# Performance work log

Hardware: AMD Instinct MI355X
Metric: run time of the kernel (lower is better)

The kernel has to match this reference:

```python
import jax, jax.numpy as jnp
import numpy as np

V, E, H, C = 50000, 300, 512, 3
B, P_LEN, H_LEN = 64, 128, 64


def _lstm(x, Wih, Whh, bih, bhh, h0, c0):
    """torch-style LSTM (gate order i,f,g,o). x: [B,T,E] -> outputs [B,T,H], hT, cT."""
    def step(carry, xt):
        h, c = carry
        g = xt @ Wih.T + h @ Whh.T + bih + bhh  # [B,4H]
        i, f, gg, o = jnp.split(g, 4, axis=-1)
        c = jax.nn.sigmoid(f) * c + jax.nn.sigmoid(i) * jnp.tanh(gg)
        h = jax.nn.sigmoid(o) * jnp.tanh(c)
        return (h, c), h
    (hT, cT), ys = jax.lax.scan(step, (h0, c0), jnp.swapaxes(x, 0, 1))
    return jnp.swapaxes(ys, 0, 1), hT, cT


def setup_inputs() -> dict:
    key = jax.random.key(0)
    ks = iter(jax.random.split(key, 32))
    n = lambda shape, s=0.05: jax.random.normal(next(ks), shape, dtype=jnp.float32) * s
    inp = {
        "premise": jax.random.randint(next(ks), (B, P_LEN), 0, V, dtype=jnp.int32),
        "hypothesis": jax.random.randint(next(ks), (B, H_LEN), 0, V, dtype=jnp.int32),
        "emb": n((V, E), 0.1),
        "Wih1": n((4 * H, E)), "Whh1": n((4 * H, H)), "bih1": n((4 * H,)), "bhh1": n((4 * H,)),
        "Wih2": n((4 * H, E)), "Whh2": n((4 * H, H)), "bih2": n((4 * H,)), "bhh2": n((4 * H,)),
        "W_y": n((H, H)), "W_h": n((H, H)), "W_r": n((H, H)), "W_t": n((H, H)),
        "w_att": n((1, H)),
        "fc1_w": n((H, H)), "fc1_b": n((H,)),
        "fc2_w": n((H, H)), "fc2_b": n((H,)),
        "fc3_w": n((C, H)), "fc3_b": n((C,)),
    }
    return inp


def reference(premise, hypothesis, emb,
              Wih1, Whh1, bih1, bhh1,
              Wih2, Whh2, bih2, bhh2,
              W_y, W_h, W_r, W_t, w_att,
              fc1_w, fc1_b, fc2_w, fc2_b, fc3_w, fc3_b):
    Bsz = premise.shape[0]
    Hd = Whh1.shape[1]
    zeros = jnp.zeros((Bsz, Hd), jnp.float32)

    # premise LSTM
    xp = emb[premise]                                   # [B,P,E]
    out_p, _, c_p = _lstm(xp, Wih1, Whh1, bih1, bhh1, zeros, zeros)
    # hypothesis LSTM initialized with (h0=0, c0=c_p)
    xh = emb[hypothesis]                                # [B,Th,E]
    out_h, hn_h, _ = _lstm(xh, Wih2, Whh2, bih2, bhh2, zeros, c_p)

    # word-by-word attention: a1 = W_y @ V^T, fixed across steps
    a1 = jnp.einsum('hj,bpj->bhp', W_y, out_p)          # [B,H,P]
    wv = w_att[0]                                       # [H]

    def att_step(r, q_t):
        # r: [B,H] attention state; q_t: [B,H] hypothesis step
        a2 = q_t @ W_h.T + r @ W_r.T                    # [B,H]
        s = jnp.einsum('h,bhp->bp', wv, jnp.tanh(a1 + a2[:, :, None]))
        scores = jax.nn.softmax(s, axis=-1)             # over premise positions
        r = jnp.einsum('bph,bp->bh', out_p, scores) + jnp.tanh(r @ W_t.T)
        return r, None

    r, _ = jax.lax.scan(att_step, zeros, jnp.swapaxes(out_h, 0, 1))

    rep = jnp.tanh(r @ fc1_w.T + fc1_b + hn_h @ fc2_w.T + fc2_b)
    return rep @ fc3_w.T + fc3_b                         # [B,C]
```

## Files before the change

kernel.cpp:

```cpp
#include <hip/hip_runtime.h>
#include <math.h>

#define BSZ 64
#define PLEN 128
#define HLEN 64
#define EDIM 300
#define HDIM 512
#define G4 2048
#define NCLS 3

#define TOFF 1000u
#define SPIN_CAP (1 << 18)

#define CR16 576
#define C16(f) ((((f) >> 5) * 36) + ((f) & 31))

__device__ __forceinline__ float sigf(float x) { return 1.0f / (1.0f + __expf(-x)); }
__device__ __forceinline__ float tanhfast(float x) { return 1.0f - 2.0f / (__expf(2.0f * x) + 1.0f); }

__device__ __forceinline__ unsigned long long aload64(const unsigned long long* p) {
    return __hip_atomic_load(p, __ATOMIC_RELAXED, __HIP_MEMORY_SCOPE_AGENT);
}
__device__ __forceinline__ void astore64(unsigned long long* p, unsigned long long v) {
    __hip_atomic_store(p, v, __ATOMIC_RELAXED, __HIP_MEMORY_SCOPE_AGENT);
}
__device__ __forceinline__ unsigned long long tpack(float v, unsigned tag) {
    return ((unsigned long long)tag << 32) | (unsigned long long)__float_as_uint(v);
}
__device__ __forceinline__ float tval(unsigned long long v) { return __uint_as_float((unsigned)v); }
__device__ __forceinline__ unsigned ttag(unsigned long long v) { return (unsigned)(v >> 32); }

__global__ __launch_bounds__(256) void ws_zero(unsigned long long* p) {
    p[(size_t)blockIdx.x * 256 + threadIdx.x] = 0ull;
}

__global__ __launch_bounds__(256) void proj_kernel(
    const int* __restrict__ toks, const float* __restrict__ emb,
    const float* __restrict__ Wih, const float* __restrict__ bih,
    const float* __restrict__ bhh, float* __restrict__ out)
{
    __shared__ float es[32 * 100];
    __shared__ float wsh[64 * 100];
    __shared__ int tks[32];
    const int m0 = blockIdx.x * 32, r0 = blockIdx.y * 64;
    const int tid = threadIdx.x;
    const int tx = tid & 15, ty = tid >> 4;
    float acc[2][4] = {{0.f, 0.f, 0.f, 0.f}, {0.f, 0.f, 0.f, 0.f}};
    if (tid < 32) tks[tid] = toks[m0 + tid];
    __syncthreads();
    for (int kc = 0; kc < 3; kc++) {
        if (kc) __syncthreads();
        for (int i = tid; i < 800; i += 256) {
            int row = i / 25, k4 = i % 25;
            ((float4*)es)[i] = ((const float4*)(emb + (size_t)tks[row] * EDIM + kc * 100))[k4];
        }
        for (int i = tid; i < 1600; i += 256) {
            int row = i / 25, k4 = i % 25;
            ((float4*)wsh)[i] = ((const float4*)(Wih + (size_t)(r0 + row) * EDIM + kc * 100))[k4];
        }
        __syncthreads();
        const float4* e0 = (const float4*)es + ty * 25;
        const float4* e1 = e0 + 16 * 25;
        const float4* w0 = (const float4*)wsh + tx * 25;
#pragma unroll
        for (int k = 0; k < 25; k++) {
            float4 ea = e0[k], eb = e1[k];
#pragma unroll
            for (int j = 0; j < 4; j++) {
                float4 w = w0[k + j * 400];
                acc[0][j] += ea.x * w.x + ea.y * w.y + ea.z * w.z + ea.w * w.w;
                acc[1][j] += eb.x * w.x + eb.y * w.y + eb.z * w.z + eb.w * w.w;
            }
        }
    }
#pragma unroll
    for (int j = 0; j < 4; j++) {
        int rr = r0 + tx + j * 16;
        float bsum = bih[rr] + bhh[rr];
        out[(size_t)(m0 + ty) * G4 + rr]      = acc[0][j] + bsum;
        out[(size_t)(m0 + ty + 16) * G4 + rr] = acc[1][j] + bsum;
    }
}

__global__ __launch_bounds__(256, 1) void lstm_coop(
    const float* __restrict__ xp, const float* __restrict__ xh,
    const float* __restrict__ Whh1, const float* __restrict__ Whh2,
    float* __restrict__ outp, float* __restrict__ outh,
    unsigned long long* __restrict__ hA, unsigned long long* __restrict__ hB,
    unsigned long long* __restrict__ hC, unsigned long long* __restrict__ hD)
{
    const int tid = threadIdx.x;
    const int ug = blockIdx.x >> 3;
    const int bg = blockIdx.x & 7;
    const int u0 = ug * 16, b0 = bg * 8;
    const int rq = tid >> 4, cc = tid & 15;

    __shared__ __align__(16) float hst[8 * CR16];
    __shared__ float gsm[64][9];

    float4 w4[32];
#pragma unroll
    for (int j = 0; j < 4; j++) {
        int rr = 4 * rq + j;
        const float4* src = (const float4*)(Whh1 +
            ((size_t)((rr >> 4) * HDIM + u0 + (rr & 15))) * HDIM) + cc * 8;
#pragma unroll
        for (int q = 0; q < 8; q++) w4[j * 8 + q] = src[q];
    }
    float creg = 0.0f;
    const int bbc = tid >> 4, uuc = tid & 15;

    for (int t = 0; t < PLEN + HLEN; t++) {
        const int layer2 = (t >= PLEN) ? 1 : 0;
        const int tloc = layer2 ? t - PLEN : t;
        const int T = layer2 ? HLEN : PLEN;
        const float* xproj = layer2 ? xh : xp;
        float* outseq = layer2 ? outh : outp;
        unsigned long long* wA = layer2 ? hC : hA;
        unsigned long long* wB = layer2 ? hD : hB;
        unsigned long long* hwr = (t & 1) ? wB : wA;
        const unsigned long long* hrd = (t & 1) ? wA : wB;

        float gi = 0.f, gf = 0.f, gg = 0.f, go = 0.f;
        if (tid < 128) {
            size_t xb = ((size_t)(b0 + bbc) * T + tloc) * G4 + u0 + uuc;
            gi = xproj[xb];        gf = xproj[xb + 512];
            gg = xproj[xb + 1024]; go = xproj[xb + 1536];
        }

        if (t == PLEN) {
#pragma unroll
            for (int j = 0; j < 4; j++) {
                int rr = 4 * rq + j;
                const float4* src = (const float4*)(Whh2 +
                    ((size_t)((rr >> 4) * HDIM + u0 + (rr & 15))) * HDIM) + cc * 8;
#pragma unroll
                for (int q = 0; q < 8; q++) w4[j * 8 + q] = src[q];
            }
        }
        const bool have_h = (tloc != 0);
        if (have_h) {
            const unsigned long long* src = hrd + (size_t)b0 * 512;
            unsigned long long v[16];
            const unsigned expt = (unsigned)t;
#pragma unroll
            for (int i = 0; i < 16; i++) v[i] = aload64(src + tid + i * 256);
            int guard = 0;
            while (true) {
                bool ok = true;
#pragma unroll
                for (int i = 0; i < 16; i++) ok &= (ttag(v[i]) == expt);
                if (__all(ok)) break;
                if (++guard > SPIN_CAP) break;
                __builtin_amdgcn_s_sleep(1);
#pragma unroll
                for (int i = 0; i < 16; i++)
                    if (ttag(v[i]) != expt) v[i] = aload64(src + tid + i * 256);
            }
            __asm__ volatile("" ::: "memory");
#pragma unroll
            for (int i = 0; i < 16; i++) {
                int idx = tid + i * 256;
                int bb = idx >> 9, u = idx & 511;
                hst[bb * CR16 + C16(u)] = tval(v[i]);
            }
            __syncthreads();
#pragma unroll 1
            for (int bb = 0; bb < 8; bb++) {
                const float* hb = &hst[bb * CR16 + cc * 36];
                float a0 = 0.f, a1 = 0.f, a2 = 0.f, a3 = 0.f;
#pragma unroll
                for (int q = 0; q < 8; q++) {
                    float4 hv = *(const float4*)(hb + 4 * q);
                    float4 x;
                    x = w4[q];      a0 += x.x * hv.x + x.y * hv.y + x.z * hv.z + x.w * hv.w;
                    x = w4[8 + q];  a1 += x.x * hv.x + x.y * hv.y + x.z * hv.z + x.w * hv.w;
                    x = w4[16 + q]; a2 += x.x * hv.x + x.y * hv.y + x.z * hv.z + x.w * hv.w;
                    x = w4[24 + q]; a3 += x.x * hv.x + x.y * hv.y + x.z * hv.z + x.w * hv.w;
                }
#pragma unroll
                for (int o = 1; o < 16; o <<= 1) {
                    a0 += __shfl_xor(a0, o);
                    a1 += __shfl_xor(a1, o);
                    a2 += __shfl_xor(a2, o);
                    a3 += __shfl_xor(a3, o);
                }
                if (cc == 0) {
                    gsm[4 * rq + 0][bb] = a0;
                    gsm[4 * rq + 1][bb] = a1;
                    gsm[4 * rq + 2][bb] = a2;
                    gsm[4 * rq + 3][bb] = a3;
                }
            }
        }
        __syncthreads();
        if (tid < 128) {
            const int b = b0 + bbc;
            if (have_h) {
                gi += gsm[uuc][bbc];
                gf += gsm[16 + uuc][bbc];
                gg += gsm[32 + uuc][bbc];
                go += gsm[48 + uuc][bbc];
            }
            float cn = sigf(gf) * creg + sigf(gi) * tanhfast(gg);
            float hn = sigf(go) * tanhfast(cn);
            creg = cn;
            astore64(hwr + (size_t)b * 512 + u0 + uuc, tpack(hn, (unsigned)(t + 1)));
            outseq[((size_t)b * T + tloc) * HDIM + u0 + uuc] = hn;
        }
    }
}

__global__ __launch_bounds__(256) void a1_kernel(
    const float* __restrict__ Wy, const float* __restrict__ outp,
    float* __restrict__ a1t)
{
    __shared__ float os[32 * 132];
    __shared__ float wsh[64 * 132];
    const int b = blockIdx.x, p0 = blockIdx.y * 32, h0 = blockIdx.z * 64;
    const int tid = threadIdx.x;
    const int tx = tid & 15, ty = tid >> 4;
    float acc[2][4] = {{0.f, 0.f, 0.f, 0.f}, {0.f, 0.f, 0.f, 0.f}};
    for (int kc = 0; kc < 4; kc++) {
        if (kc) __syncthreads();
        for (int i = tid; i < 1024; i += 256) {
            int row = i >> 5, k4 = i & 31;
            ((float4*)os)[row * 33 + k4] =
                ((const float4*)(outp + ((size_t)(b * PLEN) + p0 + row) * HDIM + kc * 128))[k4];
        }
        for (int i = tid; i < 2048; i += 256) {
            int row = i >> 5, k4 = i & 31;
            ((float4*)wsh)[row * 33 + k4] =
                ((const float4*)(Wy + (size_t)(h0 + row) * HDIM + kc * 128))[k4];
        }
        __syncthreads();
        const float4* o0 = (const float4*)os + ty * 33;
        const float4* o1 = o0 + 16 * 33;
        const float4* w0 = (const float4*)wsh + tx * 33;
#pragma unroll
        for (int k = 0; k < 32; k++) {
            float4 ea = o0[k], eb = o1[k];
#pragma unroll
            for (int j = 0; j < 4; j++) {
                float4 w = w0[k + j * 528];
                acc[0][j] += ea.x * w.x + ea.y * w.y + ea.z * w.z + ea.w * w.w;
                acc[1][j] += eb.x * w.x + eb.y * w.y + eb.z * w.z + eb.w * w.w;
            }
        }
    }
#pragma unroll
    for (int j = 0; j < 4; j++) {
        int hh = h0 + tx + j * 16;
        a1t[((size_t)b * PLEN + p0 + ty) * HDIM + hh]      = acc[0][j];
        a1t[((size_t)b * PLEN + p0 + ty + 16) * HDIM + hh] = acc[1][j];
    }
}

#define OSTR 2056
__global__ __launch_bounds__(256, 1) void att_coop(
    const float* __restrict__ outh, const float* __restrict__ a1b,
    const float* __restrict__ outp,
    const float* __restrict__ Wh, const float* __restrict__ Wr,
    const float* __restrict__ Wt, const float* __restrict__ wv,
    unsigned long long* __restrict__ a2buf, unsigned long long* __restrict__ sbuf,
    unsigned long long* __restrict__ rA, unsigned long long* __restrict__ rB)
{
    const int tid = threadIdx.x;
    const int ug = blockIdx.x >> 3;
    const int bg = blockIdx.x & 7;
    const int u0 = ug * 16, b0 = bg * 8;
    const int rq = tid >> 4, cc = tid & 15;
    const int m = rq >> 2;

    __shared__ __align__(16) float ops[8 * OSTR];
    __shared__ __align__(16) float qa[8 * CR16];
    __shared__ __align__(16) float rst[8 * CR16];
    __shared__ __align__(16) float scst[8][132];
    __shared__ float dsm[48][9];
    __shared__ float tts[16][9];
    __shared__ __align__(16) float wvs[512];

    float4 w4[32];
    if (rq < 12) {
        const float* W = (m == 0) ? Wh : ((m == 1) ? Wr : Wt);
#pragma unroll
        for (int j = 0; j < 4; j++) {
            int rr = 4 * rq + j;
            const float4* src = (const float4*)(W + (size_t)(u0 + (rr & 15)) * HDIM) + cc * 8;
#pragma unroll
            for (int q = 0; q < 8; q++) w4[j * 8 + q] = src[q];
        }
    }
    for (int i = tid; i < 128; i += 256)
        ((float4*)wvs)[i] = ((const float4*)wv)[i];

    for (int i = tid; i < 8 * 128 * 4; i += 256) {
        int bb = i >> 9;
        int rem = i & 511;
        int p = rem >> 2, q = rem & 3;
        float4 v = *((const float4*)(outp + ((size_t)(b0 + bb) * PLEN + p) * HDIM + u0) + q);
        *((float4*)(ops + bb * OSTR + p * 16) + q) = v;
    }

    const int wvid = tid >> 6, lane = tid & 63;
    const int p0g = ug * 4;
    float4 a1r[8][2];
#pragma unroll
    for (int i = 0; i < 8; i++) {
        int pr = wvid * 8 + i;
        int bb = pr >> 2, pp = pr & 3;
        const float4* src = (const float4*)(a1b + ((size_t)(b0 + bb) * PLEN + p0g + pp) * HDIM) + lane;
        a1r[i][0] = src[0];
        a1r[i][1] = src[64];
    }

    const int bbc = tid >> 4, uuc = tid & 15;

    for (int t = 0; t < HLEN; t++) {
        unsigned long long* rwr = (t & 1) ? rB : rA;
        const unsigned long long* rrd = (t & 1) ? rA : rB;

        for (int i = tid; i < 8 * 128; i += 256) {
            int bb = i >> 7, k4 = i & 127;
            float4 v = ((const float4*)(outh + ((size_t)(b0 + bb) * HLEN + t) * HDIM))[k4];
            *(float4*)&qa[bb * CR16 + (k4 >> 3) * 36 + 4 * (k4 & 7)] = v;
        }
        if (t > 0) {
            const unsigned long long* src = rrd + (size_t)b0 * 512;
            unsigned long long v[16];
            const unsigned expt = TOFF + (unsigned)(3 * t);
#pragma unroll
            for (int i = 0; i < 16; i++) v[i] = aload64(src + tid + i * 256);
            int guard = 0;
            while (true) {
                bool ok = true;
#pragma unroll
                for (int i = 0; i < 16; i++) ok &= (ttag(v[i]) == expt);
                if (__all(ok)) break;
                if (++guard > SPIN_CAP) break;
                __builtin_amdgcn_s_sleep(1);
#pragma unroll
                for (int i = 0; i < 16; i++)
                    if (ttag(v[i]) != expt) v[i] = aload64(src + tid + i * 256);
            }
            __asm__ volatile("" ::: "memory");
#pragma unroll
            for (int i = 0; i < 16; i++) {
                int idx = tid + i * 256;
                int bb = idx >> 9, u = idx & 511;
                rst[bb * CR16 + C16(u)] = tval(v[i]);
            }
        }
        __syncthreads();
        if (rq < 12 && (t > 0 || m == 0)) {
#pragma unroll 1
            for (int bb = 0; bb < 8; bb++) {
                const float* svb = ((m == 0) ? &qa[bb * CR16] : &rst[bb * CR16]) + cc * 36;
                float a0 = 0.f, a1 = 0.f, a2 = 0.f, a3 = 0.f;
#pragma unroll
                for (int q = 0; q < 8; q++) {
                    float4 sv = *(const float4*)(svb + 4 * q);
                    float4 x;
                    x = w4[q];      a0 += x.x * sv.x + x.y * sv.y + x.z * sv.z + x.w * sv.w;
                    x = w4[8 + q];  a1 += x.x * sv.x + x.y * sv.y + x.z * sv.z + x.w * sv.w;
                    x = w4[16 + q]; a2 += x.x * sv.x + x.y * sv.y + x.z * sv.z + x.w * sv.w;
                    x = w4[24 + q]; a3 += x.x * sv.x + x.y * sv.y + x.z * sv.z + x.w * sv.w;
                }
#pragma unroll
                for (int o = 1; o < 16; o <<= 1) {
                    a0 += __shfl_xor(a0, o);
                    a1 += __shfl_xor(a1, o);
                    a2 += __shfl_xor(a2, o);
                    a3 += __shfl_xor(a3, o);
                }
                if (cc == 0) {
                    dsm[4 * rq + 0][bb] = a0;
                    dsm[4 * rq + 1][bb] = a1;
                    dsm[4 * rq + 2][bb] = a2;
                    dsm[4 * rq + 3][bb] = a3;
                }
            }
        }
        __syncthreads();
        if (tid < 128) {
            float aq = dsm[uuc][bbc];
            float ar = (t > 0) ? dsm[16 + uuc][bbc] : 0.0f;
            float at = (t > 0) ? dsm[32 + uuc][bbc] : 0.0f;
            float a2v = aq + ar;
            tts[uuc][bbc] = (t > 0) ? tanhfast(at) : 0.0f;
            astore64(a2buf + (size_t)(b0 + bbc) * 512 + u0 + uuc,
                     tpack(a2v, TOFF + (unsigned)(3 * t + 1)));
        }

        {
            const unsigned long long* src = a2buf + (size_t)b0 * 512;
            unsigned long long v[16];
            const unsigned expt = TOFF + (unsigned)(3 * t + 1);
#pragma unroll
            for (int i = 0; i < 16; i++) v[i] = aload64(src + tid + i * 256);
            int guard = 0;
            while (true) {
                bool ok = true;
#pragma unroll
                for (int i = 0; i < 16; i++) ok &= (ttag(v[i]) == expt);
                if (__all(ok)) break;
                if (++guard > SPIN_CAP) break;
                __builtin_amdgcn_s_sleep(1);
#pragma unroll
                for (int i = 0; i < 16; i++)
                    if (ttag(v[i]) != expt) v[i] = aload64(src + tid + i * 256);
            }
            __asm__ volatile("" ::: "memory");
#pragma unroll
            for (int i = 0; i < 16; i++) {
                int idx = tid + i * 256;
                int bb = idx >> 9, u = idx & 511;
                qa[bb * CR16 + C16(u)] = tval(v[i]);
            }
        }
        __syncthreads();
        {
#pragma unroll 2
            for (int i = 0; i < 8; i++) {
                int pr = wvid * 8 + i;
                int bb = pr >> 2, pp = pr & 3;
                float s = 0.f;
#pragma unroll
                for (int k = 0; k < 2; k++) {
                    int h4 = lane + 64 * k;
                    float4 av = a1r[i][k];
                    float4 a2v = *(const float4*)&qa[bb * CR16 + (h4 >> 3) * 36 + 4 * (h4 & 7)];
                    float4 wv4 = ((const float4*)wvs)[h4];
                    s += wv4.x * tanhfast(av.x + a2v.x)
                       + wv4.y * tanhfast(av.y + a2v.y)
                       + wv4.z * tanhfast(av.z + a2v.z)
                       + wv4.w * tanhfast(av.w + a2v.w);
                }
#pragma unroll
                for (int o = 1; o < 64; o <<= 1) s += __shfl_xor(s, o);
                if (lane == 0)
                    astore64(sbuf + (size_t)(b0 + bb) * PLEN + p0g + pp,
                             tpack(s, TOFF + (unsigned)(3 * t + 2)));
            }
        }

        {
            const unsigned long long* src = sbuf + (size_t)b0 * 128;
            unsigned long long v[4];
            const unsigned expt = TOFF + (unsigned)(3 * t + 2);
#pragma unroll
            for (int i = 0; i < 4; i++) v[i] = aload64(src + tid + i * 256);
            int guard = 0;
            while (true) {
                bool ok = true;
#pragma unroll
                for (int i = 0; i < 4; i++) ok &= (ttag(v[i]) == expt);
                if (__all(ok)) break;
                if (++guard > SPIN_CAP) break;
                __builtin_amdgcn_s_sleep(1);
#pragma unroll
                for (int i = 0; i < 4; i++)
                    if (ttag(v[i]) != expt) v[i] = aload64(src + tid + i * 256);
            }
            __asm__ volatile("" ::: "memory");
#pragma unroll
            for (int i = 0; i < 4; i++) {
                int idx = tid + i * 256;
                int bb = idx >> 7, j = idx & 127;
                scst[bb][j] = tval(v[i]);
            }
        }
        __syncthreads();
        {
            const int bb = tid >> 5, j = tid & 31;
            float4 v = *(float4*)&scst[bb][j * 4];
            float mx = fmaxf(fmaxf(v.x, v.y), fmaxf(v.z, v.w));
#pragma unroll
            for (int o = 1; o < 32; o <<= 1) mx = fmaxf(mx, __shfl_xor(mx, o));
            float ex = __expf(v.x - mx), ey = __expf(v.y - mx);
            float ez = __expf(v.z - mx), ew = __expf(v.w - mx);
            float ssum = (ex + ey) + (ez + ew);
#pragma unroll
            for (int o = 1; o < 32; o <<= 1) ssum += __shfl_xor(ssum, o);
            float inv = 1.0f / ssum;
            float4 sc4 = make_float4(ex * inv, ey * inv, ez * inv, ew * inv);
            *(float4*)&scst[bb][j * 4] = sc4;
        }
        __syncthreads();
        if (tid < 128) {
            float acc = tts[uuc][bbc];
            const float* opb = ops + bbc * OSTR + uuc;
#pragma unroll 8
            for (int p = 0; p < PLEN; p++)
                acc += scst[bbc][p] * opb[p * 16];
            astore64(rwr + (size_t)(b0 + bbc) * 512 + u0 + uuc,
                     tpack(acc, TOFF + (unsigned)(3 * t + 3)));
        }
    }
}

__global__ __launch_bounds__(256) void final_kernel(
    const unsigned long long* __restrict__ r2, const float* __restrict__ outh,
    const float* __restrict__ fc1w, const float* __restrict__ fc1b,
    const float* __restrict__ fc2w, const float* __restrict__ fc2b,
    const float* __restrict__ fc3w, const float* __restrict__ fc3b,
    float* __restrict__ out)
{
    int b = blockIdx.x, tid = threadIdx.x;
    __shared__ float rs[HDIM], hs[HDIM], rep[HDIM], red[256];
    for (int i = tid; i < 512; i += 256)
        rs[i] = tval(r2[(size_t)b * 512 + i]);
    for (int i = tid; i < 128; i += 256)
        ((float4*)hs)[i] = ((const float4*)(outh + ((size_t)(b * HLEN + HLEN - 1)) * HDIM))[i];
    __syncthreads();
    for (int u = tid; u < HDIM; u += 256) {
        const float4* w1 = (const float4*)(fc1w + (size_t)u * HDIM);
        const float4* w2 = (const float4*)(fc2w + (size_t)u * HDIM);
        float a = 0.f, bacc = 0.f;
        for (int k = 0; k < 128; k++) {
            float4 rv = ((float4*)rs)[k], hv = ((float4*)hs)[k];
            float4 x = w1[k]; a    += rv.x * x.x + rv.y * x.y + rv.z * x.z + rv.w * x.w;
            float4 y = w2[k]; bacc += hv.x * y.x + hv.y * y.y + hv.z * y.z + hv.w * y.w;
        }
        rep[u] = tanhfast(a + fc1b[u] + bacc + fc2b[u]);
    }
    __syncthreads();
    for (int cix = 0; cix < NCLS; cix++) {
        red[tid] = rep[tid] * fc3w[(size_t)cix * HDIM + tid]
                 + rep[tid + 256] * fc3w[(size_t)cix * HDIM + tid + 256];
        __syncthreads();
        for (int off = 128; off; off >>= 1) {
            if (tid < off) red[tid] += red[tid + off];
            __syncthreads();
        }
        if (tid == 0) out[b * NCLS + cix] = red[0] + fc3b[cix];
        __syncthreads();
    }
}

extern "C" void kernel_launch(void* const* d_in, const int* in_sizes, int n_in,
                              void* d_out, int out_size, void* d_ws, size_t ws_size,
                              hipStream_t stream)
{
    const int*   premise = (const int*)d_in[0];
    const int*   hyp     = (const int*)d_in[1];
    const float* emb     = (const float*)d_in[2];
    const float* Wih1    = (const float*)d_in[3];
    const float* Whh1    = (const float*)d_in[4];
    const float* bih1    = (const float*)d_in[5];
    const float* bhh1    = (const float*)d_in[6];
    const float* Wih2    = (const float*)d_in[7];
    const float* Whh2    = (const float*)d_in[8];
    const float* bih2    = (const float*)d_in[9];
    const float* bhh2    = (const float*)d_in[10];
    const float* Wy      = (const float*)d_in[11];
    const float* Wh      = (const float*)d_in[12];
    const float* Wr      = (const float*)d_in[13];
    const float* Wt      = (const float*)d_in[14];
    const float* wv      = (const float*)d_in[15];
    const float* fc1w    = (const float*)d_in[16];
    const float* fc1b    = (const float*)d_in[17];
    const float* fc2w    = (const float*)d_in[18];
    const float* fc2b    = (const float*)d_in[19];
    const float* fc3w    = (const float*)d_in[20];
    const float* fc3b    = (const float*)d_in[21];
    float* out = (float*)d_out;

    float* ws = (float*)d_ws;
    size_t off = 0;
    float* xp    = ws + off; off += (size_t)BSZ * PLEN * G4;
    float* xh    = ws + off; off += (size_t)BSZ * HLEN * G4;
    float* outp  = ws + off; off += (size_t)BSZ * PLEN * HDIM;
    float* outhp = ws + off; off += (size_t)BSZ * HLEN * HDIM;
    float* a1b   = ws + off; off += (size_t)BSZ * HDIM * PLEN;
    unsigned long long* tbase = (unsigned long long*)(ws + off);
    unsigned long long* hAb   = tbase;
    unsigned long long* hBb   = tbase + 32768;
    unsigned long long* a2buf = tbase + 2 * 32768;
    unsigned long long* rAb   = tbase + 3 * 32768;
    unsigned long long* rBb   = tbase + 4 * 32768;
    unsigned long long* sbuf  = tbase + 5 * 32768;
    off += (size_t)(5 * 32768 + 8192) * 2;
    if (ws_size < off * sizeof(float)) return;

    ws_zero<<<dim3(672), dim3(256), 0, stream>>>(tbase);

    proj_kernel<<<dim3(BSZ * PLEN / 32, G4 / 64), dim3(256), 0, stream>>>(
        premise, emb, Wih1, bih1, bhh1, xp);
    proj_kernel<<<dim3(BSZ * HLEN / 32, G4 / 64), dim3(256), 0, stream>>>(
        hyp, emb, Wih2, bih2, bhh2, xh);

    lstm_coop<<<dim3(256), dim3(256), 0, stream>>>(
        xp, xh, Whh1, Whh2, outp, outhp, hAb, hBb, rAb, rBb);

    a1_kernel<<<dim3(BSZ, PLEN / 32, HDIM / 64), dim3(256), 0, stream>>>(Wy, outp, a1b);

    att_coop<<<dim3(256), dim3(256), 0, stream>>>(
        outhp, a1b, outp, Wh, Wr, Wt, wv, a2buf, sbuf, rAb, rBb);

    final_kernel<<<dim3(BSZ), dim3(256), 0, stream>>>(
        rBb, outhp, fc1w, fc1b, fc2w, fc2b, fc3w, fc3b, out);
}
```

Before: 3.683 ms.

## Replace per-element tagged values with per-block done counters and packed float pairs

Inter-block exchange of hidden and attention states no longer tags every float with a 32-bit step tag in a 64-bit word. Each producer block now stores packed float2 pairs, drains its stores, and bumps a per-block done counter. Consumers spin on 32 counters instead of polling 16 tagged words per thread, which halves exchange traffic and shrinks the polling work. This adds an extra barrier and a vmcnt wait per step, and correctness now depends on the relaxed-atomic store ordering being visible before the counter update.

```diff
diff --git a/kernel.cpp b/kernel.cpp
--- a/kernel.cpp
+++ b/kernel.cpp
@@ -24,11 +24,14 @@
 __device__ __forceinline__ void astore64(unsigned long long* p, unsigned long long v) {
     __hip_atomic_store(p, v, __ATOMIC_RELAXED, __HIP_MEMORY_SCOPE_AGENT);
 }
-__device__ __forceinline__ unsigned long long tpack(float v, unsigned tag) {
-    return ((unsigned long long)tag << 32) | (unsigned long long)__float_as_uint(v);
-}
-__device__ __forceinline__ float tval(unsigned long long v) { return __uint_as_float((unsigned)v); }
-__device__ __forceinline__ unsigned ttag(unsigned long long v) { return (unsigned)(v >> 32); }
+__device__ __forceinline__ unsigned long long fpack2(float lo, float hi) {
+    float2 v = make_float2(lo, hi);
+    return *(unsigned long long*)&v;
+}
+__device__ __forceinline__ float2 funpack2(unsigned long long u) {
+    union { unsigned long long u; float2 f; } c; c.u = u; return c.f;
+}
+
 
 __global__ __launch_bounds__(256) void ws_zero(unsigned long long* p) {
     p[(size_t)blockIdx.x * 256 + threadIdx.x] = 0ull;
@@ -87,7 +90,8 @@
     const float* __restrict__ Whh1, const float* __restrict__ Whh2,
     float* __restrict__ outp, float* __restrict__ outh,
     unsigned long long* __restrict__ hA, unsigned long long* __restrict__ hB,
-    unsigned long long* __restrict__ hC, unsigned long long* __restrict__ hD)
+    unsigned long long* __restrict__ hC, unsigned long long* __restrict__ hD,
+    unsigned long long* __restrict__ doneH)
 {
     const int tid = threadIdx.x;
     const int ug = blockIdx.x >> 3;
@@ -109,6 +113,7 @@
     }
     float creg = 0.0f;
     const int bbc = tid >> 4, uuc = tid & 15;
+    unsigned long long* dn = doneH + bg * 32;
 
     for (int t = 0; t < PLEN + HLEN; t++) {
         const int layer2 = (t >= PLEN) ? 1 : 0;
@@ -140,29 +145,27 @@
         }
         const bool have_h = (tloc != 0);
         if (have_h) {
-            const unsigned long long* src = hrd + (size_t)b0 * 512;
-            unsigned long long v[16];
-            const unsigned expt = (unsigned)t;
-#pragma unroll
-            for (int i = 0; i < 16; i++) v[i] = aload64(src + tid + i * 256);
-            int guard = 0;
-            while (true) {
-                bool ok = true;
-#pragma unroll
-                for (int i = 0; i < 16; i++) ok &= (ttag(v[i]) == expt);
-                if (__all(ok)) break;
-                if (++guard > SPIN_CAP) break;
-                __builtin_amdgcn_s_sleep(1);
-#pragma unroll
-                for (int i = 0; i < 16; i++)
-                    if (ttag(v[i]) != expt) v[i] = aload64(src + tid + i * 256);
-            }
+            if (tid < 32) {
+                unsigned long long v = aload64(dn + tid);
+                int guard = 0;
+                while (!__all(v >= (unsigned long long)t)) {
+                    if (++guard > SPIN_CAP) break;
+                    __builtin_amdgcn_s_sleep(1);
+                    if (v < (unsigned long long)t) v = aload64(dn + tid);
+                }
+            }
+            __syncthreads();
             __asm__ volatile("" ::: "memory");
-#pragma unroll
-            for (int i = 0; i < 16; i++) {
+            const unsigned long long* src = hrd + (size_t)b0 * 256;
+            unsigned long long v[8];
+#pragma unroll
+            for (int i = 0; i < 8; i++) v[i] = aload64(src + tid + i * 256);
+#pragma unroll
+            for (int i = 0; i < 8; i++) {
                 int idx = tid + i * 256;
-                int bb = idx >> 9, u = idx & 511;
-                hst[bb * CR16 + C16(u)] = tval(v[i]);
+                int bb = idx >> 8, j = idx & 255;
+                float2 f = funpack2(v[i]);
+                *(float2*)&hst[bb * CR16 + C16(2 * j)] = f;
             }
             __syncthreads();
 #pragma unroll 1
@@ -194,8 +197,8 @@
             }
         }
         __syncthreads();
+        float hn = 0.f;
         if (tid < 128) {
-            const int b = b0 + bbc;
             if (have_h) {
                 gi += gsm[uuc][bbc];
                 gf += gsm[16 + uuc][bbc];
@@ -203,11 +206,17 @@
                 go += gsm[48 + uuc][bbc];
             }
             float cn = sigf(gf) * creg + sigf(gi) * tanhfast(gg);
-            float hn = sigf(go) * tanhfast(cn);
+            hn = sigf(go) * tanhfast(cn);
             creg = cn;
-            astore64(hwr + (size_t)b * 512 + u0 + uuc, tpack(hn, (unsigned)(t + 1)));
-            outseq[((size_t)b * T + tloc) * HDIM + u0 + uuc] = hn;
-        }
+            float pr = __shfl_xor(hn, 1);
+            if ((uuc & 1) == 0)
+                astore64(hwr + (size_t)(b0 + bbc) * 256 + (u0 + uuc) / 2, fpack2(hn, pr));
+        }
+        __asm__ volatile("s_waitcnt vmcnt(0)" ::: "memory");
+        __syncthreads();
+        if (tid == 0) astore64(&dn[ug], (unsigned long long)(t + 1));
+        if (tid < 128)
+            outseq[((size_t)(b0 + bbc) * T + tloc) * HDIM + u0 + uuc] = hn;
     }
 }
 
@@ -263,7 +272,9 @@
     const float* __restrict__ Wh, const float* __restrict__ Wr,
     const float* __restrict__ Wt, const float* __restrict__ wv,
     unsigned long long* __restrict__ a2buf, unsigned long long* __restrict__ sbuf,
-    unsigned long long* __restrict__ rA, unsigned long long* __restrict__ rB)
+    unsigned long long* __restrict__ rA, unsigned long long* __restrict__ rB,
+    unsigned long long* __restrict__ doneA, unsigned long long* __restrict__ doneB,
+    unsigned long long* __restrict__ doneC)
 {
     const int tid = threadIdx.x;
     const int ug = blockIdx.x >> 3;
@@ -314,6 +325,9 @@
         a1r[i][1] = src[64];
     }
 
+    unsigned long long* dnA = doneA + bg * 32;
+    unsigned long long* dnB = doneB + bg * 32;
+    unsigned long long* dnC = doneC + bg * 32;
     const int bbc = tid >> 4, uuc = tid & 15;
 
     for (int t = 0; t < HLEN; t++) {
@@ -326,29 +340,28 @@
             *(float4*)&qa[bb * CR16 + (k4 >> 3) * 36 + 4 * (k4 & 7)] = v;
         }
         if (t > 0) {
-            const unsigned long long* src = rrd + (size_t)b0 * 512;
-            unsigned long long v[16];
-            const unsigned expt = TOFF + (unsigned)(3 * t);
-#pragma unroll
-            for (int i = 0; i < 16; i++) v[i] = aload64(src + tid + i * 256);
-            int guard = 0;
-            while (true) {
-                bool ok = true;
-#pragma unroll
-                for (int i = 0; i < 16; i++) ok &= (ttag(v[i]) == expt);
-                if (__all(ok)) break;
-                if (++guard > SPIN_CAP) break;
-                __builtin_amdgcn_s_sleep(1);
-#pragma unroll
-                for (int i = 0; i < 16; i++)
-                    if (ttag(v[i]) != expt) v[i] = aload64(src + tid + i * 256);
-            }
+            const unsigned long long expt = TOFF + (unsigned long long)(3 * t);
+            if (tid < 32) {
+                unsigned long long v = aload64(dnC + tid);
+                int guard = 0;
+                while (!__all(v >= expt)) {
+                    if (++guard > SPIN_CAP) break;
+                    __builtin_amdgcn_s_sleep(1);
+                    if (v < expt) v = aload64(dnC + tid);
+                }
+            }
+            __syncthreads();
             __asm__ volatile("" ::: "memory");
-#pragma unroll
-            for (int i = 0; i < 16; i++) {
+            const unsigned long long* src = rrd + (size_t)b0 * 256;
+            unsigned long long v[8];
+#pragma unroll
+            for (int i = 0; i < 8; i++) v[i] = aload64(src + tid + i * 256);
+#pragma unroll
+            for (int i = 0; i < 8; i++) {
                 int idx = tid + i * 256;
-                int bb = idx >> 9, u = idx & 511;
-                rst[bb * CR16 + C16(u)] = tval(v[i]);
+                int bb = idx >> 8, j = idx & 255;
+                float2 f = funpack2(v[i]);
+                *(float2*)&rst[bb * CR16 + C16(2 * j)] = f;
             }
         }
         __syncthreads();
@@ -388,42 +401,46 @@
             float at = (t > 0) ? dsm[32 + uuc][bbc] : 0.0f;
             float a2v = aq + ar;
             tts[uuc][bbc] = (t > 0) ? tanhfast(at) : 0.0f;
-            astore64(a2buf + (size_t)(b0 + bbc) * 512 + u0 + uuc,
-                     tpack(a2v, TOFF + (unsigned)(3 * t + 1)));
-        }
+            float pr = __shfl_xor(a2v, 1);
+            if ((uuc & 1) == 0)
+                astore64(a2buf + (size_t)(b0 + bbc) * 256 + (u0 + uuc) / 2, fpack2(a2v, pr));
+        }
+        __asm__ volatile("s_waitcnt vmcnt(0)" ::: "memory");
+        __syncthreads();
+        if (tid == 0) astore64(&dnA[ug], TOFF + (unsigned long long)(3 * t + 1));
 
         {
-            const unsigned long long* src = a2buf + (size_t)b0 * 512;
-            unsigned long long v[16];
-            const unsigned expt = TOFF + (unsigned)(3 * t + 1);
-#pragma unroll
-            for (int i = 0; i < 16; i++) v[i] = aload64(src + tid + i * 256);
-            int guard = 0;
-            while (true) {
-                bool ok = true;
-#pragma unroll
-                for (int i = 0; i < 16; i++) ok &= (ttag(v[i]) == expt);
-                if (__all(ok)) break;
-                if (++guard > SPIN_CAP) break;
-                __builtin_amdgcn_s_sleep(1);
-#pragma unroll
-                for (int i = 0; i < 16; i++)
-                    if (ttag(v[i]) != expt) v[i] = aload64(src + tid + i * 256);
-            }
+            const unsigned long long expt = TOFF + (unsigned long long)(3 * t + 1);
+            if (tid < 32) {
+                unsigned long long v = aload64(dnA + tid);
+                int guard = 0;
+                while (!__all(v >= expt)) {
+                    if (++guard > SPIN_CAP) break;
+                    __builtin_amdgcn_s_sleep(1);
+                    if (v < expt) v = aload64(dnA + tid);
+                }
+            }
+            __syncthreads();
             __asm__ volatile("" ::: "memory");
-#pragma unroll
-            for (int i = 0; i < 16; i++) {
+            const unsigned long long* src = a2buf + (size_t)b0 * 256;
+            unsigned long long v[8];
+#pragma unroll
+            for (int i = 0; i < 8; i++) v[i] = aload64(src + tid + i * 256);
+#pragma unroll
+            for (int i = 0; i < 8; i++) {
                 int idx = tid + i * 256;
-                int bb = idx >> 9, u = idx & 511;
-                qa[bb * CR16 + C16(u)] = tval(v[i]);
+                int bb = idx >> 8, j = idx & 255;
+                float2 f = funpack2(v[i]);
+                *(float2*)&qa[bb * CR16 + C16(2 * j)] = f;
             }
         }
         __syncthreads();
         {
+            float s8[8];
 #pragma unroll 2
             for (int i = 0; i < 8; i++) {
                 int pr = wvid * 8 + i;
-                int bb = pr >> 2, pp = pr & 3;
+                int bb = pr >> 2;
                 float s = 0.f;
 #pragma unroll
                 for (int k = 0; k < 2; k++) {
@@ -438,36 +455,42 @@
                 }
 #pragma unroll
                 for (int o = 1; o < 64; o <<= 1) s += __shfl_xor(s, o);
-                if (lane == 0)
-                    astore64(sbuf + (size_t)(b0 + bb) * PLEN + p0g + pp,
-                             tpack(s, TOFF + (unsigned)(3 * t + 2)));
-            }
-        }
+                s8[i] = s;
+            }
+            if (lane == 0) {
+#pragma unroll
+                for (int i = 0; i < 8; i += 2) {
+                    int pr = wvid * 8 + i;
+                    int bb = pr >> 2, pp = pr & 3;
+                    astore64(sbuf + (size_t)(b0 + bb) * 64 + ug * 2 + (pp >> 1),
+                             fpack2(s8[i], s8[i + 1]));
+                }
+            }
+        }
+        __asm__ volatile("s_waitcnt vmcnt(0)" ::: "memory");
+        __syncthreads();
+        if (tid == 0) astore64(&dnB[ug], TOFF + (unsigned long long)(3 * t + 2));
 
         {
-            const unsigned long long* src = sbuf + (size_t)b0 * 128;
-            unsigned long long v[4];
-            const unsigned expt = TOFF + (unsigned)(3 * t + 2);
-#pragma unroll
-            for (int i = 0; i < 4; i++) v[i] = aload64(src + tid + i * 256);
-            int guard = 0;
-            while (true) {
-                bool ok = true;
-#pragma unroll
-                for (int i = 0; i < 4; i++) ok &= (ttag(v[i]) == expt);
-                if (__all(ok)) break;
-                if (++guard > SPIN_CAP) break;
-                __builtin_amdgcn_s_sleep(1);
-#pragma unroll
-                for (int i = 0; i < 4; i++)
-                    if (ttag(v[i]) != expt) v[i] = aload64(src + tid + i * 256);
-            }
+            const unsigned long long expt = TOFF + (unsigned long long)(3 * t + 2);
+            if (tid < 32) {
+                unsigned long long v = aload64(dnB + tid);
+                int guard = 0;
+                while (!__all(v >= expt)) {
+                    if (++guard > SPIN_CAP) break;
+                    __builtin_amdgcn_s_sleep(1);
+                    if (v < expt) v = aload64(dnB + tid);
+                }
+            }
+            __syncthreads();
             __asm__ volatile("" ::: "memory");
-#pragma unroll
-            for (int i = 0; i < 4; i++) {
+            const unsigned long long* src = sbuf + (size_t)b0 * 64;
+#pragma unroll
+            for (int i = 0; i < 2; i++) {
                 int idx = tid + i * 256;
-                int bb = idx >> 7, j = idx & 127;
-                scst[bb][j] = tval(v[i]);
+                int bb = idx >> 6, j = idx & 63;
+                float2 f = funpack2(aload64(src + bb * 64 + j));
+                *(float2*)&scst[bb][2 * j] = f;
             }
         }
         __syncthreads();
@@ -493,9 +516,13 @@
 #pragma unroll 8
             for (int p = 0; p < PLEN; p++)
                 acc += scst[bbc][p] * opb[p * 16];
-            astore64(rwr + (size_t)(b0 + bbc) * 512 + u0 + uuc,
-                     tpack(acc, TOFF + (unsigned)(3 * t + 3)));
-        }
+            float pr = __shfl_xor(acc, 1);
+            if ((uuc & 1) == 0)
+                astore64(rwr + (size_t)(b0 + bbc) * 256 + (u0 + uuc) / 2, fpack2(acc, pr));
+        }
+        __asm__ volatile("s_waitcnt vmcnt(0)" ::: "memory");
+        __syncthreads();
+        if (tid == 0) astore64(&dnC[ug], TOFF + (unsigned long long)(3 * t + 3));
     }
 }
 
@@ -508,8 +535,10 @@
 {
     int b = blockIdx.x, tid = threadIdx.x;
     __shared__ float rs[HDIM], hs[HDIM], rep[HDIM], red[256];
-    for (int i = tid; i < 512; i += 256)
-        rs[i] = tval(r2[(size_t)b * 512 + i]);
+    {
+        float2 f = funpack2(r2[(size_t)b * 256 + tid]);
+        rs[2 * tid] = f.x; rs[2 * tid + 1] = f.y;
+    }
     for (int i = tid; i < 128; i += 256)
         ((float4*)hs)[i] = ((const float4*)(outh + ((size_t)(b * HLEN + HLEN - 1)) * HDIM))[i];
     __syncthreads();
@@ -575,15 +604,19 @@
     float* a1b   = ws + off; off += (size_t)BSZ * HDIM * PLEN;
     unsigned long long* tbase = (unsigned long long*)(ws + off);
     unsigned long long* hAb   = tbase;
-    unsigned long long* hBb   = tbase + 32768;
-    unsigned long long* a2buf = tbase + 2 * 32768;
-    unsigned long long* rAb   = tbase + 3 * 32768;
-    unsigned long long* rBb   = tbase + 4 * 32768;
-    unsigned long long* sbuf  = tbase + 5 * 32768;
-    off += (size_t)(5 * 32768 + 8192) * 2;
+    unsigned long long* hBb   = tbase + 16384;
+    unsigned long long* hCb   = tbase + 2 * 16384;
+    unsigned long long* hDb   = tbase + 3 * 16384;
+    unsigned long long* a2b   = tbase + 4 * 16384;
+    unsigned long long* sbb   = tbase + 5 * 16384;
+    unsigned long long* dnH   = tbase + 5 * 16384 + 4096;
+    unsigned long long* dnA   = dnH + 256;
+    unsigned long long* dnB   = dnA + 256;
+    unsigned long long* dnC   = dnB + 256;
+    off += (size_t)(5 * 16384 + 4096 + 1024) * 2;
     if (ws_size < off * sizeof(float)) return;
 
-    ws_zero<<<dim3(672), dim3(256), 0, stream>>>(tbase);
+    ws_zero<<<dim3(4), dim3(256), 0, stream>>>(dnH);
 
     proj_kernel<<<dim3(BSZ * PLEN / 32, G4 / 64), dim3(256), 0, stream>>>(
         premise, emb, Wih1, bih1, bhh1, xp);
@@ -591,13 +624,13 @@
         hyp, emb, Wih2, bih2, bhh2, xh);
 
     lstm_coop<<<dim3(256), dim3(256), 0, stream>>>(
-        xp, xh, Whh1, Whh2, outp, outhp, hAb, hBb, rAb, rBb);
+        xp, xh, Whh1, Whh2, outp, outhp, hAb, hBb, hCb, hDb, dnH);
 
     a1_kernel<<<dim3(BSZ, PLEN / 32, HDIM / 64), dim3(256), 0, stream>>>(Wy, outp, a1b);
 
     att_coop<<<dim3(256), dim3(256), 0, stream>>>(
-        outhp, a1b, outp, Wh, Wr, Wt, wv, a2buf, sbuf, rAb, rBb);
+        outhp, a1b, outp, Wh, Wr, Wt, wv, a2b, sbb, hCb, hDb, dnA, dnB, dnC);
 
     final_kernel<<<dim3(BSZ), dim3(256), 0, stream>>>(
-        rBb, outhp, fc1w, fc1b, fc2w, fc2b, fc3w, fc3b, out);
-}
+        hDb, outhp, fc1w, fc1b, fc2w, fc2b, fc3w, fc3b, out);
+}
```

New measurement: 3.442 ms. 6.5% less time.
